# Kernel optimization log

Measured on AMD Instinct MI355X. Metric: run time of the kernel, lower is better.

The kernel has to match this reference:

```python
import jax, jax.numpy as jnp
import numpy as np

SEQ, D_IN, H, D_OUT = 8192, 256, 2048, 64


def setup_inputs() -> dict:
    key = jax.random.key(0)
    ks = jax.random.split(key, 9)
    s = 1.0 / np.sqrt(H)  # torch LSTM/Linear init scale
    u = lambda k, shape: jax.random.uniform(k, shape, jnp.float32, -s, s)
    return {
        "x": jax.random.normal(ks[0], (SEQ, D_IN), jnp.float32),
        "hprev": jax.random.normal(ks[1], (1, 1, H), jnp.float32),
        "cprev": jax.random.normal(ks[2], (1, 1, H), jnp.float32),
        "W_ih": u(ks[3], (4 * H, D_IN)),   # gate order: i, f, g, o
        "W_hh": u(ks[4], (4 * H, H)),
        "b_ih": u(ks[5], (4 * H,)),
        "b_hh": u(ks[6], (4 * H,)),
        "W_fc": u(ks[7], (D_OUT, H)),
        "b_fc": u(ks[8], (D_OUT,)),
    }


def _lstm_forward(x, h0, c0, W_ih, W_hh, b_ih, b_hh, W_fc, b_fc):
    # precompute input contributions for all timesteps: [T, 4H]
    xg = x @ W_ih.T + (b_ih + b_hh)
    W_hh_T = W_hh.T  # [H, 4H]

    def step(carry, xg_t):
        h, c = carry
        z = xg_t + h @ W_hh_T  # [4H]
        i, f, g, o = jnp.split(z, 4)
        i = jax.nn.sigmoid(i)
        f = jax.nn.sigmoid(f)
        g = jnp.tanh(g)
        o = jax.nn.sigmoid(o)
        c = f * c + i * g
        h = o * jnp.tanh(c)
        return (h, c), h

    (hT, cT), hs = jax.lax.scan(step, (h0, c0), xg)
    out = jax.nn.sigmoid(hs @ W_fc.T + b_fc)  # [T, D_OUT]
    return out, hT, cT


def reference(x, hprev, cprev, W_ih, W_hh, b_ih, b_hh, W_fc, b_fc):
    out, hT, cT = _lstm_forward(
        x, hprev[0, 0], cprev[0, 0], W_ih, W_hh, b_ih, b_hh, W_fc, b_fc
    )
    return out, hT[None, None, :], cT[None, None, :]
```

## Files before the change

### kernel.cpp

```cpp
#include <hip/hip_runtime.h>
#include <hip/hip_bf16.h>
#include <stdint.h>

typedef __fp16 f16x2 __attribute__((ext_vector_type(2)));
typedef __fp16 f16x8 __attribute__((ext_vector_type(8)));
typedef unsigned long long ull;

#define SEQ  8192
#define HDIM 2048
#define DIN  256
#define DOUT 64

__device__ __forceinline__ f16x2 pk(float lo, float hi) {
    return __builtin_amdgcn_cvt_pkrtz(lo, hi);
}
__device__ __forceinline__ f16x2 pk2(float2 v) { return pk(v.x, v.y); }
__device__ __forceinline__ uint32_t h2u(f16x2 h) { return __builtin_bit_cast(uint32_t, h); }
__device__ __forceinline__ float sigf(float x) { return 1.0f / (1.0f + __expf(-x)); }

__device__ __forceinline__ int skH(int j) { return j + 4 * (j >> 7); }
__device__ __forceinline__ int skX(int j) { return j + 4 * (j >> 4); }

__global__ void __launch_bounds__(256, 1)
lstm_persist(const float2* __restrict__ x2,
             const float2* __restrict__ hprev2,
             const float*  __restrict__ cprev,
             const float*  __restrict__ wih,
             const float*  __restrict__ whh,
             const float*  __restrict__ bih,
             const float*  __restrict__ bhh,
             const float2* __restrict__ wfc2,
             const float*  __restrict__ bfc,
             float* __restrict__ out,
             uint32_t* __restrict__ hs_w,
             ull* __restrict__ htag)
{
    const int tid = threadIdx.x;
    const int b   = blockIdx.x;
    const int w   = tid >> 6;
    const int u   = (tid >> 3) & 7;
    const int c   = tid & 7;

    __shared__ __align__(16) uint32_t smem[12672];
    uint32_t* ldsH0 = smem;
    uint32_t* ldsH1 = smem + 1056;
    uint32_t* ldsX  = smem + 2112;
    float*    zbuf  = (float*)(smem + 2272);
    uint32_t* hsl = smem;
    uint32_t* wfl = smem + 4224;

    uint32_t* hs_priv = hs_w + (size_t)b * 32 * 1024;

    const int r = w * 2048 + 8 * b + u;
    f16x2 wh[128];
    {
        const float4* p = (const float4*)(whh + (size_t)r * 2048 + 256 * c);
#pragma unroll
        for (int q = 0; q < 64; ++q) {
            float4 v = p[q];
            wh[2*q+0] = pk(v.x, v.y);
            wh[2*q+1] = pk(v.z, v.w);
        }
    }
    f16x2 wx[16];
    {
        const float4* p = (const float4*)(wih + (size_t)r * 256 + 32 * c);
#pragma unroll
        for (int q = 0; q < 8; ++q) {
            float4 v = p[q];
            wx[2*q+0] = pk(v.x, v.y);
            wx[2*q+1] = pk(v.z, v.w);
        }
    }
#pragma unroll
    for (int k = 0; k < 4; ++k) {
        int j = tid + 256 * k;
        ldsH0[skH(j)] = h2u(pk2(hprev2[j]));
    }
    if (tid < 128) ldsX[skX(tid)] = h2u(pk2(x2[tid]));

    float cloc = 0.f, hloc = 0.f, b0 = 0.f, b1 = 0.f, b2 = 0.f, b3 = 0.f;
    if (tid < 8) {
        int j = 8 * b + tid;
        cloc = cprev[j];
        b0 = bih[j]        + bhh[j];
        b1 = bih[2048 + j] + bhh[2048 + j];
        b2 = bih[4096 + j] + bhh[4096 + j];
        b3 = bih[6144 + j] + bhh[6144 + j];
    }
    const ull deadline = __builtin_amdgcn_s_memrealtime() + 60000000ull;
    __syncthreads();

    for (int t = 0; t < SEQ; ++t) {
        uint32_t* ldsH = (t & 1) ? ldsH1 : ldsH0;

        float accs[8];
#pragma unroll
        for (int q = 0; q < 8; ++q) accs[q] = 0.f;
        {
            const f16x8* xp = (const f16x8*)(ldsX + 20 * c);
#pragma unroll
            for (int q = 0; q < 4; ++q) {
                f16x8 xv = xp[q];
#pragma unroll
                for (int d = 0; d < 4; ++d) {
                    f16x2 hv = {xv[2*d], xv[2*d+1]};
                    int idx = 4 * q + d;
                    accs[idx & 7] = __builtin_amdgcn_fdot2(wx[idx], hv, accs[idx & 7], false);
                }
            }
        }
        float2 xw = {0.f, 0.f};
        const bool xl = (tid < 128) && (t + 1 < SEQ);
        if (xl) xw = x2[(size_t)(t + 1) * 128 + tid];

        if (t > 0) {
            const ull* tag = htag + (size_t)(t & 1) * 1024;
            uint32_t pay[4] = {0, 0, 0, 0};
            unsigned got = 0;
            while (got != 0xFu) {
#pragma unroll
                for (int k = 0; k < 4; ++k) {
                    if (!(got & (1u << k))) {
                        ull v = __hip_atomic_load(tag + (tid + 256 * k),
                                                  __ATOMIC_RELAXED, __HIP_MEMORY_SCOPE_AGENT);
                        if ((uint32_t)(v >> 32) == (uint32_t)t) {
                            pay[k] = (uint32_t)v;
                            got |= (1u << k);
                        }
                    }
                }
                if (got != 0xFu) {
                    if (__builtin_amdgcn_s_memrealtime() > deadline) got = 0xFu;
                    __builtin_amdgcn_s_sleep(1);
                }
            }
            const bool save = (((t - 1) >> 5) == b);
#pragma unroll
            for (int k = 0; k < 4; ++k) {
                int j = tid + 256 * k;
                ldsH[skH(j)] = pay[k];
                if (save) hs_priv[(size_t)((t - 1) & 31) * 1024 + j] = pay[k];
            }
        }
        __syncthreads();
        if (xl) ldsX[skX(tid)] = h2u(pk2(xw));

        {
            const f16x8* hp = (const f16x8*)(ldsH + 132 * c);
#pragma unroll
            for (int q = 0; q < 32; ++q) {
                f16x8 hv8 = hp[q];
#pragma unroll
                for (int d = 0; d < 4; ++d) {
                    f16x2 hh = {hv8[2*d], hv8[2*d+1]};
                    int idx = 4 * q + d;
                    accs[idx & 7] = __builtin_amdgcn_fdot2(wh[idx], hh, accs[idx & 7], false);
                }
            }
        }
        float acc = ((accs[0] + accs[1]) + (accs[2] + accs[3]))
                  + ((accs[4] + accs[5]) + (accs[6] + accs[7]));
        acc += __shfl_xor(acc, 1);
        acc += __shfl_xor(acc, 2);
        acc += __shfl_xor(acc, 4);
        if (c == 0) zbuf[w * 8 + u] = acc;
        __syncthreads();

        if (tid < 8) {
            float zi = zbuf[tid]      + b0;
            float zf = zbuf[8  + tid] + b1;
            float zg = zbuf[16 + tid] + b2;
            float zo = zbuf[24 + tid] + b3;
            float ig = sigf(zi), fg = sigf(zf), og = sigf(zo);
            float gg = tanhf(zg);
            cloc = fg * cloc + ig * gg;
            hloc = og * tanhf(cloc);
            float hot = __shfl_xor(hloc, 1);
            if ((tid & 1) == 0) {
                uint32_t pay = h2u(pk(hloc, hot));
                ull tv = ((ull)(uint32_t)(t + 1) << 32) | (ull)pay;
                __hip_atomic_store(htag + ((size_t)((t + 1) & 1) * 1024 + 4 * b + (tid >> 1)),
                                   tv, __ATOMIC_RELAXED, __HIP_MEMORY_SCOPE_AGENT);
            }
        }
    }

    if (tid < 8) {
        out[(size_t)SEQ * DOUT + 8 * b + tid]        = hloc;
        out[(size_t)SEQ * DOUT + HDIM + 8 * b + tid] = cloc;
    }

    if (b == 255) {
        uint32_t pay[4] = {0, 0, 0, 0};
        unsigned got = 0;
        while (got != 0xFu) {
#pragma unroll
            for (int k = 0; k < 4; ++k) {
                if (!(got & (1u << k))) {
                    ull v = __hip_atomic_load(htag + (tid + 256 * k),
                                              __ATOMIC_RELAXED, __HIP_MEMORY_SCOPE_AGENT);
                    if ((uint32_t)(v >> 32) == 8192u) {
                        pay[k] = (uint32_t)v;
                        got |= (1u << k);
                    }
                }
            }
            if (got != 0xFu) {
                if (__builtin_amdgcn_s_memrealtime() > deadline) got = 0xFu;
                __builtin_amdgcn_s_sleep(1);
            }
        }
#pragma unroll
        for (int k = 0; k < 4; ++k)
            hs_priv[(size_t)31 * 1024 + tid + 256 * k] = pay[k];
    }
    __syncthreads();

    const int cc = tid & 63;
    const int rg = tid >> 6;
    const float bo = bfc[cc];
    float fca[8];
#pragma unroll
    for (int q = 0; q < 8; ++q) fca[q] = 0.f;

    for (int ch = 0; ch < 8; ++ch) {
#pragma unroll
        for (int i = 0; i < 16; ++i) {
            int idx = tid + 256 * i;
            int rr = idx >> 7, kp = idx & 127;
            hsl[rr * 132 + kp] = hs_priv[(size_t)rr * 1024 + ch * 128 + kp];
        }
#pragma unroll
        for (int i = 0; i < 32; ++i) {
            int idx = tid + 256 * i;
            int c2 = idx >> 7, kp = idx & 127;
            wfl[c2 * 132 + kp] = h2u(pk2(wfc2[(size_t)c2 * 1024 + ch * 128 + kp]));
        }
        __syncthreads();
#pragma unroll 4
        for (int k4 = 0; k4 < 32; ++k4) {
            f16x8 wv = *(const f16x8*)(wfl + cc * 132 + 4 * k4);
#pragma unroll
            for (int q = 0; q < 8; ++q) {
                f16x8 hv = *(const f16x8*)(hsl + (rg * 8 + q) * 132 + 4 * k4);
#pragma unroll
                for (int d = 0; d < 4; ++d) {
                    f16x2 a  = {hv[2*d], hv[2*d+1]};
                    f16x2 bb = {wv[2*d], wv[2*d+1]};
                    fca[q] = __builtin_amdgcn_fdot2(a, bb, fca[q], false);
                }
            }
        }
        __syncthreads();
    }
#pragma unroll
    for (int q = 0; q < 8; ++q) {
        size_t row = (size_t)32 * b + rg * 8 + q;
        out[row * DOUT + cc] = sigf(fca[q] + bo);
    }
}

extern "C" void kernel_launch(void* const* d_in, const int* in_sizes, int n_in,
                              void* d_out, int out_size, void* d_ws, size_t ws_size,
                              hipStream_t stream) {
    const float2* x2     = (const float2*)d_in[0];
    const float2* hprev2 = (const float2*)d_in[1];
    const float*  cprev  = (const float*)d_in[2];
    const float*  wih    = (const float*)d_in[3];
    const float*  whh    = (const float*)d_in[4];
    const float*  bih    = (const float*)d_in[5];
    const float*  bhh    = (const float*)d_in[6];
    const float2* wfc2   = (const float2*)d_in[7];
    const float*  bfc    = (const float*)d_in[8];
    float*        out    = (float*)d_out;

    uint32_t* hs_w = (uint32_t*)d_ws;
    ull*      htag = (ull*)((char*)d_ws + (size_t)SEQ * 1024 * 4);

    lstm_persist<<<dim3(256), dim3(256), 0, stream>>>(
        x2, hprev2, cprev, wih, whh, bih, bhh, wfc2, bfc,
        out, hs_w, htag);
}
```

Before: 24.74 ms.

## Compute LSTM gates within each wavefront and replicate h broadcast tags

```diff
diff --git a/kernel.cpp b/kernel.cpp
--- a/kernel.cpp
+++ b/kernel.cpp
@@ -1,5 +1,4 @@
 #include <hip/hip_runtime.h>
-#include <hip/hip_bf16.h>
 #include <stdint.h>
 
 typedef __fp16 f16x2 __attribute__((ext_vector_type(2)));
@@ -10,6 +9,7 @@
 #define HDIM 2048
 #define DIN  256
 #define DOUT 64
+#define NREP 4
 
 __device__ __forceinline__ f16x2 pk(float lo, float hi) {
     return __builtin_amdgcn_cvt_pkrtz(lo, hi);
@@ -17,6 +17,7 @@
 __device__ __forceinline__ f16x2 pk2(float2 v) { return pk(v.x, v.y); }
 __device__ __forceinline__ uint32_t h2u(f16x2 h) { return __builtin_bit_cast(uint32_t, h); }
 __device__ __forceinline__ float sigf(float x) { return 1.0f / (1.0f + __expf(-x)); }
+__device__ __forceinline__ float tanh_fast(float x) { return 2.0f * sigf(2.0f * x) - 1.0f; }
 
 __device__ __forceinline__ int skH(int j) { return j + 4 * (j >> 7); }
 __device__ __forceinline__ int skX(int j) { return j + 4 * (j >> 4); }
@@ -37,37 +38,39 @@
 {
     const int tid = threadIdx.x;
     const int b   = blockIdx.x;
-    const int w   = tid >> 6;
-    const int u   = (tid >> 3) & 7;
-    const int c   = tid & 7;
+    const int wv  = tid >> 6;
+    const int l   = tid & 63;
+    const int g   = l >> 4;
+    const int p   = (l >> 3) & 1;
+    const int c   = l & 7;
 
     __shared__ __align__(16) uint32_t smem[12672];
     uint32_t* ldsH0 = smem;
     uint32_t* ldsH1 = smem + 1056;
     uint32_t* ldsX  = smem + 2112;
-    float*    zbuf  = (float*)(smem + 2272);
     uint32_t* hsl = smem;
     uint32_t* wfl = smem + 4224;
 
     uint32_t* hs_priv = hs_w + (size_t)b * 32 * 1024;
 
-    const int r = w * 2048 + 8 * b + u;
+    const int unit = 8 * b + 2 * wv + p;
+    const int r    = g * 2048 + unit;
     f16x2 wh[128];
     {
-        const float4* p = (const float4*)(whh + (size_t)r * 2048 + 256 * c);
+        const float4* ptr = (const float4*)(whh + (size_t)r * 2048 + 256 * c);
 #pragma unroll
         for (int q = 0; q < 64; ++q) {
-            float4 v = p[q];
+            float4 v = ptr[q];
             wh[2*q+0] = pk(v.x, v.y);
             wh[2*q+1] = pk(v.z, v.w);
         }
     }
     f16x2 wx[16];
     {
-        const float4* p = (const float4*)(wih + (size_t)r * 256 + 32 * c);
+        const float4* ptr = (const float4*)(wih + (size_t)r * 256 + 32 * c);
 #pragma unroll
         for (int q = 0; q < 8; ++q) {
-            float4 v = p[q];
+            float4 v = ptr[q];
             wx[2*q+0] = pk(v.x, v.y);
             wx[2*q+1] = pk(v.z, v.w);
         }
@@ -79,15 +82,9 @@
     }
     if (tid < 128) ldsX[skX(tid)] = h2u(pk2(x2[tid]));
 
-    float cloc = 0.f, hloc = 0.f, b0 = 0.f, b1 = 0.f, b2 = 0.f, b3 = 0.f;
-    if (tid < 8) {
-        int j = 8 * b + tid;
-        cloc = cprev[j];
-        b0 = bih[j]        + bhh[j];
-        b1 = bih[2048 + j] + bhh[2048 + j];
-        b2 = bih[4096 + j] + bhh[4096 + j];
-        b3 = bih[6144 + j] + bhh[6144 + j];
-    }
+    float cloc = cprev[unit];
+    float hloc = 0.f;
+    const float bsum = bih[r] + bhh[r];
     const ull deadline = __builtin_amdgcn_s_memrealtime() + 60000000ull;
     __syncthreads();
 
@@ -115,9 +112,10 @@
         if (xl) xw = x2[(size_t)(t + 1) * 128 + tid];
 
         if (t > 0) {
-            const ull* tag = htag + (size_t)(t & 1) * 1024;
+            const ull* tag = htag + (size_t)(b & (NREP - 1)) * 2048 + (size_t)(t & 1) * 1024;
             uint32_t pay[4] = {0, 0, 0, 0};
             unsigned got = 0;
+            int spins = 0;
             while (got != 0xFu) {
 #pragma unroll
                 for (int k = 0; k < 4; ++k) {
@@ -131,8 +129,10 @@
                     }
                 }
                 if (got != 0xFu) {
-                    if (__builtin_amdgcn_s_memrealtime() > deadline) got = 0xFu;
-                    __builtin_amdgcn_s_sleep(1);
+                    if (spins++ > 0) {
+                        if (__builtin_amdgcn_s_memrealtime() > deadline) got = 0xFu;
+                        __builtin_amdgcn_s_sleep(1);
+                    }
                 }
             }
             const bool save = (((t - 1) >> 5) == b);
@@ -164,41 +164,43 @@
         acc += __shfl_xor(acc, 1);
         acc += __shfl_xor(acc, 2);
         acc += __shfl_xor(acc, 4);
-        if (c == 0) zbuf[w * 8 + u] = acc;
-        __syncthreads();
-
-        if (tid < 8) {
-            float zi = zbuf[tid]      + b0;
-            float zf = zbuf[8  + tid] + b1;
-            float zg = zbuf[16 + tid] + b2;
-            float zo = zbuf[24 + tid] + b3;
-            float ig = sigf(zi), fg = sigf(zf), og = sigf(zo);
-            float gg = tanhf(zg);
-            cloc = fg * cloc + ig * gg;
-            hloc = og * tanhf(cloc);
-            float hot = __shfl_xor(hloc, 1);
-            if ((tid & 1) == 0) {
-                uint32_t pay = h2u(pk(hloc, hot));
-                ull tv = ((ull)(uint32_t)(t + 1) << 32) | (ull)pay;
-                __hip_atomic_store(htag + ((size_t)((t + 1) & 1) * 1024 + 4 * b + (tid >> 1)),
-                                   tv, __ATOMIC_RELAXED, __HIP_MEMORY_SCOPE_AGENT);
-            }
-        }
-    }
-
-    if (tid < 8) {
-        out[(size_t)SEQ * DOUT + 8 * b + tid]        = hloc;
-        out[(size_t)SEQ * DOUT + HDIM + 8 * b + tid] = cloc;
+
+        float z = acc + bsum;
+        const bool isg = (g == 2);
+        float s  = sigf(isg ? 2.0f * z : z);
+        float val = isg ? (2.0f * s - 1.0f) : s;
+        const int p8 = l & 8;
+        float iv = __shfl(val, p8 + 0);
+        float fv = __shfl(val, p8 + 16);
+        float gv = __shfl(val, p8 + 32);
+        float ov = __shfl(val, p8 + 48);
+        cloc = fv * cloc + iv * gv;
+        hloc = ov * tanh_fast(cloc);
+
+        float h0 = __shfl(hloc, 0);
+        float h1 = __shfl(hloc, 8);
+        uint32_t pay = h2u(pk(h0, h1));
+        if (l < NREP) {
+            ull tv = ((ull)(uint32_t)(t + 1) << 32) | (ull)pay;
+            __hip_atomic_store(htag + (size_t)l * 2048 + (size_t)((t + 1) & 1) * 1024 + 4 * b + wv,
+                               tv, __ATOMIC_RELAXED, __HIP_MEMORY_SCOPE_AGENT);
+        }
+    }
+
+    if ((l & 55) == 0) {
+        out[(size_t)SEQ * DOUT + unit - g * 0]       = hloc;
+        out[(size_t)SEQ * DOUT + HDIM + unit]        = cloc;
     }
 
     if (b == 255) {
+        const ull* tag = htag + (size_t)(255 & (NREP - 1)) * 2048;
         uint32_t pay[4] = {0, 0, 0, 0};
         unsigned got = 0;
         while (got != 0xFu) {
 #pragma unroll
             for (int k = 0; k < 4; ++k) {
                 if (!(got & (1u << k))) {
-                    ull v = __hip_atomic_load(htag + (tid + 256 * k),
+                    ull v = __hip_atomic_load(tag + (tid + 256 * k),
                                               __ATOMIC_RELAXED, __HIP_MEMORY_SCOPE_AGENT);
                     if ((uint32_t)(v >> 32) == 8192u) {
                         pay[k] = (uint32_t)v;
@@ -240,14 +242,14 @@
         __syncthreads();
 #pragma unroll 4
         for (int k4 = 0; k4 < 32; ++k4) {
-            f16x8 wv = *(const f16x8*)(wfl + cc * 132 + 4 * k4);
+            f16x8 wvv = *(const f16x8*)(wfl + cc * 132 + 4 * k4);
 #pragma unroll
             for (int q = 0; q < 8; ++q) {
                 f16x8 hv = *(const f16x8*)(hsl + (rg * 8 + q) * 132 + 4 * k4);
 #pragma unroll
                 for (int d = 0; d < 4; ++d) {
                     f16x2 a  = {hv[2*d], hv[2*d+1]};
-                    f16x2 bb = {wv[2*d], wv[2*d+1]};
+                    f16x2 bb = {wvv[2*d], wvv[2*d+1]};
                     fca[q] = __builtin_amdgcn_fdot2(a, bb, fca[q], false);
                 }
             }
```

Result: faster. 24.08 ms (-2.7%).
